# Kernel optimization log

Hardware: AMD Instinct MI355X
Metric: run time of the kernel (lower is better)

## Reference

```python
import jax, jax.numpy as jnp
import numpy as np

N_SRC1, N_DST1, N_DST2 = 200000, 50000, 10000
E1, E2 = 2000000, 400000
IN_F, H_F, N_CLS = 128, 256, 47


def setup_inputs() -> dict:
    key = jax.random.key(0)
    ks = jax.random.split(key, 10)
    x = jax.random.normal(ks[0], (N_SRC1, IN_F), dtype=jnp.float32)
    W_self1 = jax.random.normal(ks[1], (IN_F, H_F), dtype=jnp.float32) * (1.0 / np.sqrt(IN_F))
    W_neigh1 = jax.random.normal(ks[2], (IN_F, H_F), dtype=jnp.float32) * (1.0 / np.sqrt(IN_F))
    b1 = jnp.zeros((H_F,), dtype=jnp.float32)
    W_self2 = jax.random.normal(ks[3], (H_F, N_CLS), dtype=jnp.float32) * (1.0 / np.sqrt(H_F))
    W_neigh2 = jax.random.normal(ks[4], (H_F, N_CLS), dtype=jnp.float32) * (1.0 / np.sqrt(H_F))
    b2 = jnp.zeros((N_CLS,), dtype=jnp.float32)
    src1 = jax.random.randint(ks[5], (E1,), 0, N_SRC1, dtype=jnp.int64)
    dst1 = jnp.sort(jax.random.randint(ks[6], (E1,), 0, N_DST1, dtype=jnp.int64))
    src2 = jax.random.randint(ks[7], (E2,), 0, N_DST1, dtype=jnp.int64)
    dst2 = jnp.sort(jax.random.randint(ks[8], (E2,), 0, N_DST2, dtype=jnp.int64))
    return {"x": x, "W_self1": W_self1, "W_neigh1": W_neigh1, "b1": b1,
            "W_self2": W_self2, "W_neigh2": W_neigh2, "b2": b2,
            "src1": src1, "dst1": dst1, "src2": src2, "dst2": dst2,
            "n_dst1": N_DST1, "n_dst2": N_DST2}


def _sage_mean(h_src, h_dst, src, dst, n_dst, W_self, W_neigh, b):
    # mean neighbor aggregation: gather src feats, segment-sum onto dst, divide by in-degree
    msum = jax.ops.segment_sum(h_src[src], dst, num_segments=n_dst)  # [n_dst, F]
    deg = jax.ops.segment_sum(jnp.ones(src.shape, h_src.dtype), dst, num_segments=n_dst)
    h_neigh = msum / jnp.maximum(deg, 1.0)[:, None]
    return h_dst @ W_self + h_neigh @ W_neigh + b


def reference(x, W_self1, W_neigh1, b1, W_self2, W_neigh2, b2,
              src1, dst1, src2, dst2, n_dst1, n_dst2):
    # layer 1 (dst nodes are the prefix of src nodes, DGL MFG convention)
    h = _sage_mean(x, x[:n_dst1], src1, dst1, n_dst1, W_self1, W_neigh1, b1)
    h = jax.nn.relu(h)  # dropout = identity (eval mode)
    # layer 2
    out = _sage_mean(h, h[:n_dst2], src2, dst2, n_dst2, W_self2, W_neigh2, b2)
    return out
```

## Files before the change

kernel.cpp:

```cpp
#include <hip/hip_runtime.h>

constexpr int N_DST1 = 50000;
constexpr int N_DST2 = 10000;
constexpr int E1     = 2000000;
constexpr int E2     = 400000;
constexpr int IN_F   = 128;
constexpr int H_F    = 256;
constexpr int N_CLS  = 47;

constexpr size_t RP1_OFF = 0;
constexpr size_t RP2_OFF = 204800;
constexpr size_t BPS_OFF = 245760;
constexpr size_t BPN_OFF = 311296;
constexpr size_t BP2_OFF = 376832;
constexpr size_t X8_OFF  = 430080;
constexpr size_t HN1_OFF = 26030080;
constexpr size_t HB_OFF  = 38830080;
constexpr size_t H8_OFF  = 64430080;
constexpr size_t HN2_OFF = 77230080;

using f32x4  = __attribute__((ext_vector_type(4))) float;
using f32x2  = __attribute__((ext_vector_type(2))) float;
using short8 = __attribute__((ext_vector_type(8))) short;

__device__ __forceinline__ ushort f2bf(float f) {
    union { float f; unsigned u; } v; v.f = f;
    unsigned u = v.u;
    return (ushort)((u + 0x7fffu + ((u >> 16) & 1u)) >> 16);
}

constexpr int CAST_BLKS = 200000 * IN_F / 8 / 256;
constexpr int PACK_BLKS = 44;
constexpr int RP_BLKS   = (N_DST1 + N_DST2 + 2 + 255) / 256;

__global__ __launch_bounds__(256) void setup_all(
    const float* __restrict__ x, unsigned char* __restrict__ x8,
    const float* __restrict__ Ws1, const float* __restrict__ Wn1,
    const float* __restrict__ Ws2, const float* __restrict__ Wn2,
    ushort* __restrict__ bps, ushort* __restrict__ bpn, ushort* __restrict__ bp2,
    const int* __restrict__ dst1, const int* __restrict__ dst2,
    int* __restrict__ rp1, int* __restrict__ rp2) {
    int b = blockIdx.x;
    if (b < CAST_BLKS) {
        int i = b * 256 + threadIdx.x;
        float4 v0 = ((const float4*)x)[2 * i];
        float4 v1 = ((const float4*)x)[2 * i + 1];
        int p0 = __builtin_amdgcn_cvt_pk_fp8_f32(v0.x, v0.y, 0, false);
        p0     = __builtin_amdgcn_cvt_pk_fp8_f32(v0.z, v0.w, p0, true);
        int p1 = __builtin_amdgcn_cvt_pk_fp8_f32(v1.x, v1.y, 0, false);
        p1     = __builtin_amdgcn_cvt_pk_fp8_f32(v1.z, v1.w, p1, true);
        uint2 o; o.x = (unsigned)p0; o.y = (unsigned)p1;
        ((uint2*)x8)[i] = o;
    } else if (b < CAST_BLKS + PACK_BLKS) {
        int pb = b - CAST_BLKS;
        if (pb < 32) {
            const float* W = (pb < 16) ? Ws1 : Wn1;
            ushort* P      = (pb < 16) ? bps : bpn;
            int idx = (pb & 15) * 256 + threadIdx.x;
            int lane = idx & 63, kb = (idx >> 6) & 3, nb = idx >> 8;
            int n  = nb * 16 + (lane & 15);
            int k0 = kb * 32 + ((lane >> 4) * 8);
            ushort tmp[8];
#pragma unroll
            for (int j = 0; j < 8; ++j) tmp[j] = f2bf(W[(k0 + j) * H_F + n]);
            ((uint4*)P)[idx] = *(uint4*)tmp;
        } else {
            int idx = (pb - 32) * 256 + threadIdx.x;
            if (idx < 3072) {
                int lane = idx & 63, rem = idx >> 6;
                int nb = rem % 3, kb = rem / 3;
                int col = nb * 16 + (lane & 15);
                int k0  = (kb & 7) * 32 + ((lane >> 4) * 8);
                const float* W = (kb < 8) ? Ws2 : Wn2;
                ushort tmp[8];
#pragma unroll
                for (int j = 0; j < 8; ++j)
                    tmp[j] = (col < N_CLS) ? f2bf(W[(k0 + j) * N_CLS + col]) : (ushort)0;
                ((uint4*)bp2)[(kb * 3 + nb) * 64 + lane] = *(uint4*)tmp;
            }
        }
    } else {
        int idx = (b - CAST_BLKS - PACK_BLKS) * 256 + threadIdx.x;
        const int* dst; int* rp; int E; int target;
        if (idx <= N_DST1) { dst = dst1; rp = rp1; E = E1; target = idx; }
        else if (idx <= N_DST1 + 1 + N_DST2) {
            dst = dst2; rp = rp2; E = E2; target = idx - (N_DST1 + 1);
        } else return;
        int lo = 0, hi = E;
        while (lo < hi) {
            int mid = (lo + hi) >> 1;
            if (dst[mid] < target) lo = mid + 1; else hi = mid;
        }
        rp[target] = lo;
    }
}

__global__ __launch_bounds__(256) void agg1b(const unsigned char* __restrict__ x8,
                                             const int* __restrict__ src,
                                             const int* __restrict__ rp,
                                             ushort* __restrict__ hn) {
    int t = threadIdx.x & 63;
    int d = blockIdx.x * 4 + (threadIdx.x >> 6);
    int s = rp[d], e = rp[d + 1];
    int deg = e - s;
    const uint4* x4 = (const uint4*)x8;
    int g = t >> 3, c = t & 7;
    f32x2 a2[8] = {};
    auto accv = [&](uint4 v) {
        a2[0] += __builtin_amdgcn_cvt_pk_f32_fp8((int)v.x, false);
        a2[1] += __builtin_amdgcn_cvt_pk_f32_fp8((int)v.x, true);
        a2[2] += __builtin_amdgcn_cvt_pk_f32_fp8((int)v.y, false);
        a2[3] += __builtin_amdgcn_cvt_pk_f32_fp8((int)v.y, true);
        a2[4] += __builtin_amdgcn_cvt_pk_f32_fp8((int)v.z, false);
        a2[5] += __builtin_amdgcn_cvt_pk_f32_fp8((int)v.z, true);
        a2[6] += __builtin_amdgcn_cvt_pk_f32_fp8((int)v.w, false);
        a2[7] += __builtin_amdgcn_cvt_pk_f32_fp8((int)v.w, true);
    };
    for (int b0 = s; b0 < e; b0 += 64) {
        int nb = min(64, e - b0);
        int idx = 0;
        if (t < nb) idx = src[b0 + t];
        int nfull = nb >> 3;
        int j = 0;
        for (; j + 4 <= nfull; j += 4) {
            int e0 = __shfl(idx, (j + 0) * 8 + g);
            int e1 = __shfl(idx, (j + 1) * 8 + g);
            int e2 = __shfl(idx, (j + 2) * 8 + g);
            int e3 = __shfl(idx, (j + 3) * 8 + g);
            uint4 v0 = x4[(size_t)e0 * 8 + c];
            uint4 v1 = x4[(size_t)e1 * 8 + c];
            uint4 v2 = x4[(size_t)e2 * 8 + c];
            uint4 v3 = x4[(size_t)e3 * 8 + c];
            accv(v0); accv(v1); accv(v2); accv(v3);
        }
        for (; j < nfull; ++j) {
            int e0 = __shfl(idx, j * 8 + g);
            uint4 v = x4[(size_t)e0 * 8 + c];
            accv(v);
        }
        int rem = nb & 7;
        int er = __shfl(idx, (nfull * 8 + g) & 63);
        if (g < rem) {
            uint4 v = x4[(size_t)er * 8 + c];
            accv(v);
        }
    }
#pragma unroll
    for (int q = 0; q < 8; ++q) {
#pragma unroll
        for (int h = 0; h < 2; ++h) {
            float av = a2[q][h];
            av += __shfl_xor(av, 8);
            av += __shfl_xor(av, 16);
            av += __shfl_xor(av, 32);
            a2[q][h] = av;
        }
    }
    if (t < 8) {
        float inv = 1.f / fmaxf((float)deg, 1.f);
        unsigned o[8];
#pragma unroll
        for (int p = 0; p < 8; ++p)
            o[p] = (unsigned)f2bf(a2[p][0] * inv) |
                   ((unsigned)f2bf(a2[p][1] * inv) << 16);
        uint4* hrow = (uint4*)hn + (size_t)d * 16 + t * 2;
        hrow[0] = make_uint4(o[0], o[1], o[2], o[3]);
        hrow[1] = make_uint4(o[4], o[5], o[6], o[7]);
    }
}

__global__ __launch_bounds__(256) void agg2b(const unsigned char* __restrict__ h8,
                                             const int* __restrict__ src,
                                             const int* __restrict__ rp,
                                             ushort* __restrict__ hn) {
    int t = threadIdx.x & 63;
    int d = blockIdx.x * 4 + (threadIdx.x >> 6);
    int s = rp[d], e = rp[d + 1];
    int deg = e - s;
    const uint4* h4 = (const uint4*)h8;
    int g = t >> 4, c = t & 15;
    f32x2 a2[8] = {};
    auto accv = [&](uint4 v) {
        a2[0] += __builtin_amdgcn_cvt_pk_f32_fp8((int)v.x, false);
        a2[1] += __builtin_amdgcn_cvt_pk_f32_fp8((int)v.x, true);
        a2[2] += __builtin_amdgcn_cvt_pk_f32_fp8((int)v.y, false);
        a2[3] += __builtin_amdgcn_cvt_pk_f32_fp8((int)v.y, true);
        a2[4] += __builtin_amdgcn_cvt_pk_f32_fp8((int)v.z, false);
        a2[5] += __builtin_amdgcn_cvt_pk_f32_fp8((int)v.z, true);
        a2[6] += __builtin_amdgcn_cvt_pk_f32_fp8((int)v.w, false);
        a2[7] += __builtin_amdgcn_cvt_pk_f32_fp8((int)v.w, true);
    };
    for (int b0 = s; b0 < e; b0 += 64) {
        int nb = min(64, e - b0);
        int idx = 0;
        if (t < nb) idx = src[b0 + t];
        int nfull = nb >> 2;
        int j = 0;
        for (; j + 4 <= nfull; j += 4) {
            int e0 = __shfl(idx, (j + 0) * 4 + g);
            int e1 = __shfl(idx, (j + 1) * 4 + g);
            int e2 = __shfl(idx, (j + 2) * 4 + g);
            int e3 = __shfl(idx, (j + 3) * 4 + g);
            uint4 v0 = h4[(size_t)e0 * 16 + c];
            uint4 v1 = h4[(size_t)e1 * 16 + c];
            uint4 v2 = h4[(size_t)e2 * 16 + c];
            uint4 v3 = h4[(size_t)e3 * 16 + c];
            accv(v0); accv(v1); accv(v2); accv(v3);
        }
        for (; j < nfull; ++j) {
            int e0 = __shfl(idx, j * 4 + g);
            uint4 v = h4[(size_t)e0 * 16 + c];
            accv(v);
        }
        int rem = nb & 3;
        int er = __shfl(idx, (nfull * 4 + g) & 63);
        if (g < rem) {
            uint4 v = h4[(size_t)er * 16 + c];
            accv(v);
        }
    }
#pragma unroll
    for (int q = 0; q < 8; ++q) {
#pragma unroll
        for (int h = 0; h < 2; ++h) {
            float av = a2[q][h];
            av += __shfl_xor(av, 16);
            av += __shfl_xor(av, 32);
            a2[q][h] = av;
        }
    }
    if (t < 16) {
        float inv = 1.f / fmaxf((float)deg, 1.f);
        unsigned o[8];
#pragma unroll
        for (int p = 0; p < 8; ++p)
            o[p] = (unsigned)f2bf(a2[p][0] * inv) |
                   ((unsigned)f2bf(a2[p][1] * inv) << 16);
        uint4* hrow = (uint4*)hn + (size_t)d * 32 + t * 2;
        hrow[0] = make_uint4(o[0], o[1], o[2], o[3]);
        hrow[1] = make_uint4(o[4], o[5], o[6], o[7]);
    }
}

__global__ __launch_bounds__(256) void gemm1_mfma(
    const float* __restrict__ x, const ushort* __restrict__ hn1,
    const ushort* __restrict__ BpS, const ushort* __restrict__ BpN,
    const float* __restrict__ b1, ushort* __restrict__ hb,
    unsigned char* __restrict__ h8) {
    int tid = threadIdx.x;
    int wave = tid >> 6, lane = tid & 63;
    int m0 = blockIdx.x * 16;
    int nb0 = wave * 4;
    int mloc = lane & 15;
    int mrow = m0 + mloc;
    int koff = (lane >> 4) * 8;

    const float*  Af = x   + (size_t)mrow * IN_F;
    const ushort* Ah = hn1 + (size_t)mrow * IN_F;
    short8 a0[4], a1[4];
#pragma unroll
    for (int kb = 0; kb < 4; ++kb) {
        float4 q0 = *(const float4*)(Af + kb * 32 + koff);
        float4 q1 = *(const float4*)(Af + kb * 32 + koff + 4);
        a0[kb][0] = (short)f2bf(q0.x); a0[kb][1] = (short)f2bf(q0.y);
        a0[kb][2] = (short)f2bf(q0.z); a0[kb][3] = (short)f2bf(q0.w);
        a0[kb][4] = (short)f2bf(q1.x); a0[kb][5] = (short)f2bf(q1.y);
        a0[kb][6] = (short)f2bf(q1.z); a0[kb][7] = (short)f2bf(q1.w);
        a1[kb] = *(const short8*)(Ah + kb * 32 + koff);
    }

    f32x4 acc[4];
#pragma unroll
    for (int nb = 0; nb < 4; ++nb) acc[nb] = (f32x4){0.f, 0.f, 0.f, 0.f};

#pragma unroll
    for (int kb = 0; kb < 4; ++kb)
#pragma unroll
        for (int nb = 0; nb < 4; ++nb) {
            short8 b = *(const short8*)(BpS + ((size_t)((nb0 + nb) * 4 + kb) * 64 + lane) * 8);
            acc[nb] = __builtin_amdgcn_mfma_f32_16x16x32_bf16(a0[kb], b, acc[nb], 0, 0, 0);
        }
#pragma unroll
    for (int kb = 0; kb < 4; ++kb)
#pragma unroll
        for (int nb = 0; nb < 4; ++nb) {
            short8 b = *(const short8*)(BpN + ((size_t)((nb0 + nb) * 4 + kb) * 64 + lane) * 8);
            acc[nb] = __builtin_amdgcn_mfma_f32_16x16x32_bf16(a1[kb], b, acc[nb], 0, 0, 0);
        }

    int crow0 = m0 + (lane >> 4) * 4;
    int ccol  = lane & 15;
#pragma unroll
    for (int nb = 0; nb < 4; ++nb) {
        size_t col = (size_t)(nb0 + nb) * 16 + ccol;
        float bias = b1[col];
#pragma unroll
        for (int r = 0; r < 4; ++r) {
            int row = crow0 + r;
            float v = fmaxf(acc[nb][r] + bias, 0.f);
            int p = __builtin_amdgcn_cvt_pk_fp8_f32(v, v, 0, false);
            h8[(size_t)row * H_F + col] = (unsigned char)(p & 0xff);
            if (row < N_DST2) hb[(size_t)row * H_F + col] = f2bf(v);
        }
    }
}

__global__ __launch_bounds__(256) void gemm2_mfma(
    const ushort* __restrict__ hb, const ushort* __restrict__ hn2,
    const ushort* __restrict__ P2, const float* __restrict__ b2,
    float* __restrict__ out) {
    int tid = threadIdx.x;
    int wave = tid >> 6, lane = tid & 63;
    int m0 = (blockIdx.x * 4 + wave) * 16;
    if (m0 >= N_DST2) return;
    int mrow = m0 + (lane & 15);
    int koff = (lane >> 4) * 8;

    f32x4 acc[3];
#pragma unroll
    for (int nb = 0; nb < 3; ++nb) acc[nb] = (f32x4){0.f, 0.f, 0.f, 0.f};

#pragma unroll
    for (int kb = 0; kb < 16; ++kb) {
        const ushort* A = (kb < 8)
            ? (hb  + (size_t)mrow * H_F + kb * 32 + koff)
            : (hn2 + (size_t)mrow * H_F + (kb - 8) * 32 + koff);
        short8 a = *(const short8*)A;
#pragma unroll
        for (int nb = 0; nb < 3; ++nb) {
            short8 b = *(const short8*)(P2 + ((size_t)(kb * 3 + nb) * 64 + lane) * 8);
            acc[nb] = __builtin_amdgcn_mfma_f32_16x16x32_bf16(a, b, acc[nb], 0, 0, 0);
        }
    }
    int crow0 = m0 + (lane >> 4) * 4;
    int ccol  = lane & 15;
#pragma unroll
    for (int nb = 0; nb < 3; ++nb) {
        int col = nb * 16 + ccol;
        if (col < N_CLS) {
            float bias = b2[col];
#pragma unroll
            for (int r = 0; r < 4; ++r)
                out[(size_t)(crow0 + r) * N_CLS + col] = acc[nb][r] + bias;
        }
    }
}

extern "C" void kernel_launch(void* const* d_in, const int* in_sizes, int n_in,
                              void* d_out, int out_size, void* d_ws, size_t ws_size,
                              hipStream_t stream) {
    const float* x   = (const float*)d_in[0];
    const float* Ws1 = (const float*)d_in[1];
    const float* Wn1 = (const float*)d_in[2];
    const float* b1  = (const float*)d_in[3];
    const float* Ws2 = (const float*)d_in[4];
    const float* Wn2 = (const float*)d_in[5];
    const float* b2  = (const float*)d_in[6];
    const int* src1  = (const int*)d_in[7];
    const int* dst1  = (const int*)d_in[8];
    const int* src2  = (const int*)d_in[9];
    const int* dst2  = (const int*)d_in[10];
    float* out = (float*)d_out;

    char* ws = (char*)d_ws;
    int*           rp1 = (int*)(ws + RP1_OFF);
    int*           rp2 = (int*)(ws + RP2_OFF);
    ushort*        bps = (ushort*)(ws + BPS_OFF);
    ushort*        bpn = (ushort*)(ws + BPN_OFF);
    ushort*        bp2 = (ushort*)(ws + BP2_OFF);
    unsigned char* x8  = (unsigned char*)(ws + X8_OFF);
    ushort*        hn1 = (ushort*)(ws + HN1_OFF);
    ushort*        hb  = (ushort*)(ws + HB_OFF);
    unsigned char* h8  = (unsigned char*)(ws + H8_OFF);
    ushort*        hn2 = (ushort*)(ws + HN2_OFF);

    setup_all<<<CAST_BLKS + PACK_BLKS + RP_BLKS, 256, 0, stream>>>(
        x, x8, Ws1, Wn1, Ws2, Wn2, bps, bpn, bp2, dst1, dst2, rp1, rp2);
    agg1b<<<N_DST1 / 4, 256, 0, stream>>>(x8, src1, rp1, hn1);
    gemm1_mfma<<<N_DST1 / 16, 256, 0, stream>>>(x, hn1, bps, bpn, b1, hb, h8);
    agg2b<<<N_DST2 / 4, 256, 0, stream>>>(h8, src2, rp2, hn2);
    gemm2_mfma<<<(N_DST2 / 16 + 3) / 4, 256, 0, stream>>>(hb, hn2, bp2, b2, out);
}
```

Measured before the change: 281.7 us.

## Project layer-2 features before neighbor aggregation to shrink gather width

Uses linearity of the mean to apply W_neigh2 to every layer-1 output inside gemm1, producing a 64-wide bf16 projection per node. Layer-2 aggregation then gathers 128-byte rows instead of 256-byte fp8 rows, and gemm2 adds the aggregated projection in its epilogue instead of running a second K=256 pass. In exchange gemm1 takes on extra MFMA work, shared-memory staging and a cross-wave reduction for all 50k rows, and the projected values are rounded to bf16 before they are summed.

```diff
diff --git a/kernel.cpp b/kernel.cpp
--- a/kernel.cpp
+++ b/kernel.cpp
@@ -16,8 +16,8 @@
 constexpr size_t X8_OFF  = 430080;
 constexpr size_t HN1_OFF = 26030080;
 constexpr size_t HB_OFF  = 38830080;
-constexpr size_t H8_OFF  = 64430080;
-constexpr size_t HN2_OFF = 77230080;
+constexpr size_t Y_OFF   = 64430080;
+constexpr size_t YAGG_OFF= 77230080;
 
 using f32x4  = __attribute__((ext_vector_type(4))) float;
 using f32x2  = __attribute__((ext_vector_type(2))) float;
@@ -27,6 +27,13 @@
     union { float f; unsigned u; } v; v.f = f;
     unsigned u = v.u;
     return (ushort)((u + 0x7fffu + ((u >> 16) & 1u)) >> 16);
+}
+
+__device__ __forceinline__ float bflo(unsigned x) {
+    union { unsigned q; float f; } w; w.q = x << 16; return w.f;
+}
+__device__ __forceinline__ float bfhi(unsigned x) {
+    union { unsigned q; float f; } w; w.q = x & 0xffff0000u; return w.f;
 }
 
 constexpr int CAST_BLKS = 200000 * IN_F / 8 / 256;
@@ -169,84 +176,13 @@
     }
 }
 
-__global__ __launch_bounds__(256) void agg2b(const unsigned char* __restrict__ h8,
-                                             const int* __restrict__ src,
-                                             const int* __restrict__ rp,
-                                             ushort* __restrict__ hn) {
-    int t = threadIdx.x & 63;
-    int d = blockIdx.x * 4 + (threadIdx.x >> 6);
-    int s = rp[d], e = rp[d + 1];
-    int deg = e - s;
-    const uint4* h4 = (const uint4*)h8;
-    int g = t >> 4, c = t & 15;
-    f32x2 a2[8] = {};
-    auto accv = [&](uint4 v) {
-        a2[0] += __builtin_amdgcn_cvt_pk_f32_fp8((int)v.x, false);
-        a2[1] += __builtin_amdgcn_cvt_pk_f32_fp8((int)v.x, true);
-        a2[2] += __builtin_amdgcn_cvt_pk_f32_fp8((int)v.y, false);
-        a2[3] += __builtin_amdgcn_cvt_pk_f32_fp8((int)v.y, true);
-        a2[4] += __builtin_amdgcn_cvt_pk_f32_fp8((int)v.z, false);
-        a2[5] += __builtin_amdgcn_cvt_pk_f32_fp8((int)v.z, true);
-        a2[6] += __builtin_amdgcn_cvt_pk_f32_fp8((int)v.w, false);
-        a2[7] += __builtin_amdgcn_cvt_pk_f32_fp8((int)v.w, true);
-    };
-    for (int b0 = s; b0 < e; b0 += 64) {
-        int nb = min(64, e - b0);
-        int idx = 0;
-        if (t < nb) idx = src[b0 + t];
-        int nfull = nb >> 2;
-        int j = 0;
-        for (; j + 4 <= nfull; j += 4) {
-            int e0 = __shfl(idx, (j + 0) * 4 + g);
-            int e1 = __shfl(idx, (j + 1) * 4 + g);
-            int e2 = __shfl(idx, (j + 2) * 4 + g);
-            int e3 = __shfl(idx, (j + 3) * 4 + g);
-            uint4 v0 = h4[(size_t)e0 * 16 + c];
-            uint4 v1 = h4[(size_t)e1 * 16 + c];
-            uint4 v2 = h4[(size_t)e2 * 16 + c];
-            uint4 v3 = h4[(size_t)e3 * 16 + c];
-            accv(v0); accv(v1); accv(v2); accv(v3);
-        }
-        for (; j < nfull; ++j) {
-            int e0 = __shfl(idx, j * 4 + g);
-            uint4 v = h4[(size_t)e0 * 16 + c];
-            accv(v);
-        }
-        int rem = nb & 3;
-        int er = __shfl(idx, (nfull * 4 + g) & 63);
-        if (g < rem) {
-            uint4 v = h4[(size_t)er * 16 + c];
-            accv(v);
-        }
-    }
-#pragma unroll
-    for (int q = 0; q < 8; ++q) {
-#pragma unroll
-        for (int h = 0; h < 2; ++h) {
-            float av = a2[q][h];
-            av += __shfl_xor(av, 16);
-            av += __shfl_xor(av, 32);
-            a2[q][h] = av;
-        }
-    }
-    if (t < 16) {
-        float inv = 1.f / fmaxf((float)deg, 1.f);
-        unsigned o[8];
-#pragma unroll
-        for (int p = 0; p < 8; ++p)
-            o[p] = (unsigned)f2bf(a2[p][0] * inv) |
-                   ((unsigned)f2bf(a2[p][1] * inv) << 16);
-        uint4* hrow = (uint4*)hn + (size_t)d * 32 + t * 2;
-        hrow[0] = make_uint4(o[0], o[1], o[2], o[3]);
-        hrow[1] = make_uint4(o[4], o[5], o[6], o[7]);
-    }
-}
-
 __global__ __launch_bounds__(256) void gemm1_mfma(
     const float* __restrict__ x, const ushort* __restrict__ hn1,
     const ushort* __restrict__ BpS, const ushort* __restrict__ BpN,
-    const float* __restrict__ b1, ushort* __restrict__ hb,
-    unsigned char* __restrict__ h8) {
+    const ushort* __restrict__ P2, const float* __restrict__ b1,
+    ushort* __restrict__ hb, ushort* __restrict__ y) {
+    __shared__ ushort lh[16][264];
+    __shared__ f32x4 pred[3][3][64];
     int tid = threadIdx.x;
     int wave = tid >> 6, lane = tid & 63;
     int m0 = blockIdx.x * 16;
@@ -288,7 +224,7 @@
             acc[nb] = __builtin_amdgcn_mfma_f32_16x16x32_bf16(a1[kb], b, acc[nb], 0, 0, 0);
         }
 
-    int crow0 = m0 + (lane >> 4) * 4;
+    int crow0 = (lane >> 4) * 4;
     int ccol  = lane & 15;
 #pragma unroll
     for (int nb = 0; nb < 4; ++nb) {
@@ -298,15 +234,112 @@
         for (int r = 0; r < 4; ++r) {
             int row = crow0 + r;
             float v = fmaxf(acc[nb][r] + bias, 0.f);
-            int p = __builtin_amdgcn_cvt_pk_fp8_f32(v, v, 0, false);
-            h8[(size_t)row * H_F + col] = (unsigned char)(p & 0xff);
-            if (row < N_DST2) hb[(size_t)row * H_F + col] = f2bf(v);
-        }
+            ushort bv = f2bf(v);
+            lh[row][col] = bv;
+            if (m0 + row < N_DST2) hb[(size_t)(m0 + row) * H_F + col] = bv;
+        }
+    }
+    __syncthreads();
+
+    f32x4 acc2[3];
+#pragma unroll
+    for (int q = 0; q < 3; ++q) acc2[q] = (f32x4){0.f, 0.f, 0.f, 0.f};
+#pragma unroll
+    for (int i = 0; i < 2; ++i) {
+        int kb = wave * 2 + i;
+        short8 a = *(const short8*)&lh[mloc][kb * 32 + koff];
+#pragma unroll
+        for (int q = 0; q < 3; ++q) {
+            short8 b = *(const short8*)(P2 + ((size_t)((8 + kb) * 3 + q) * 64 + lane) * 8);
+            acc2[q] = __builtin_amdgcn_mfma_f32_16x16x32_bf16(a, b, acc2[q], 0, 0, 0);
+        }
+    }
+    if (wave != 0) {
+#pragma unroll
+        for (int q = 0; q < 3; ++q) pred[wave - 1][q][lane] = acc2[q];
+    }
+    __syncthreads();
+    if (wave == 0) {
+#pragma unroll
+        for (int q = 0; q < 3; ++q) {
+            f32x4 v = acc2[q];
+            v += pred[0][q][lane]; v += pred[1][q][lane]; v += pred[2][q][lane];
+#pragma unroll
+            for (int r = 0; r < 4; ++r)
+                y[(size_t)(m0 + crow0 + r) * 64 + q * 16 + ccol] = f2bf(v[r]);
+        }
+#pragma unroll
+        for (int r = 0; r < 4; ++r)
+            y[(size_t)(m0 + crow0 + r) * 64 + 48 + ccol] = 0;
+    }
+}
+
+__global__ __launch_bounds__(256) void agg2y(const ushort* __restrict__ y,
+                                             const int* __restrict__ src,
+                                             const int* __restrict__ rp,
+                                             float* __restrict__ yagg) {
+    int t = threadIdx.x & 63;
+    int d = blockIdx.x * 4 + (threadIdx.x >> 6);
+    int s = rp[d], e = rp[d + 1];
+    int deg = e - s;
+    const uint4* y4 = (const uint4*)y;
+    int g = t >> 3, c = t & 7;
+    float a[8] = {};
+    auto accv = [&](uint4 v) {
+        a[0] += bflo(v.x); a[1] += bfhi(v.x);
+        a[2] += bflo(v.y); a[3] += bfhi(v.y);
+        a[4] += bflo(v.z); a[5] += bfhi(v.z);
+        a[6] += bflo(v.w); a[7] += bfhi(v.w);
+    };
+    for (int b0 = s; b0 < e; b0 += 64) {
+        int nb = min(64, e - b0);
+        int idx = 0;
+        if (t < nb) idx = src[b0 + t];
+        int nfull = nb >> 3;
+        int j = 0;
+        for (; j + 4 <= nfull; j += 4) {
+            int e0 = __shfl(idx, (j + 0) * 8 + g);
+            int e1 = __shfl(idx, (j + 1) * 8 + g);
+            int e2 = __shfl(idx, (j + 2) * 8 + g);
+            int e3 = __shfl(idx, (j + 3) * 8 + g);
+            uint4 v0 = y4[(size_t)e0 * 8 + c];
+            uint4 v1 = y4[(size_t)e1 * 8 + c];
+            uint4 v2 = y4[(size_t)e2 * 8 + c];
+            uint4 v3 = y4[(size_t)e3 * 8 + c];
+            accv(v0); accv(v1); accv(v2); accv(v3);
+        }
+        for (; j < nfull; ++j) {
+            int e0 = __shfl(idx, j * 8 + g);
+            uint4 v = y4[(size_t)e0 * 8 + c];
+            accv(v);
+        }
+        int rem = nb & 7;
+        int er = __shfl(idx, (nfull * 8 + g) & 63);
+        if (g < rem) {
+            uint4 v = y4[(size_t)er * 8 + c];
+            accv(v);
+        }
+    }
+#pragma unroll
+    for (int q = 0; q < 8; ++q) {
+        float av = a[q];
+        av += __shfl_xor(av, 8);
+        av += __shfl_xor(av, 16);
+        av += __shfl_xor(av, 32);
+        a[q] = av;
+    }
+    if (t < 8) {
+        float inv = 1.f / fmaxf((float)deg, 1.f);
+        float4 o0 = make_float4(a[0] * inv, a[1] * inv, a[2] * inv, a[3] * inv);
+        float4 o1 = make_float4(a[4] * inv, a[5] * inv, a[6] * inv, a[7] * inv);
+        float4* row = (float4*)(yagg + (size_t)d * 64 + t * 8);
+        row[0] = o0;
+        row[1] = o1;
     }
 }
 
 __global__ __launch_bounds__(256) void gemm2_mfma(
-    const ushort* __restrict__ hb, const ushort* __restrict__ hn2,
+    const ushort* __restrict__ hb, const float* __restrict__ yagg,
     const ushort* __restrict__ P2, const float* __restrict__ b2,
     float* __restrict__ out) {
     int tid = threadIdx.x;
@@ -321,11 +354,8 @@
     for (int nb = 0; nb < 3; ++nb) acc[nb] = (f32x4){0.f, 0.f, 0.f, 0.f};
 
 #pragma unroll
-    for (int kb = 0; kb < 16; ++kb) {
-        const ushort* A = (kb < 8)
-            ? (hb  + (size_t)mrow * H_F + kb * 32 + koff)
-            : (hn2 + (size_t)mrow * H_F + (kb - 8) * 32 + koff);
-        short8 a = *(const short8*)A;
+    for (int kb = 0; kb < 8; ++kb) {
+        short8 a = *(const short8*)(hb + (size_t)mrow * H_F + kb * 32 + koff);
 #pragma unroll
         for (int nb = 0; nb < 3; ++nb) {
             short8 b = *(const short8*)(P2 + ((size_t)(kb * 3 + nb) * 64 + lane) * 8);
@@ -340,8 +370,10 @@
         if (col < N_CLS) {
             float bias = b2[col];
 #pragma unroll
-            for (int r = 0; r < 4; ++r)
-                out[(size_t)(crow0 + r) * N_CLS + col] = acc[nb][r] + bias;
+            for (int r = 0; r < 4; ++r) {
+                float nv = yagg[(size_t)(crow0 + r) * 64 + col];
+                out[(size_t)(crow0 + r) * N_CLS + col] = acc[nb][r] + nv + bias;
+            }
         }
     }
 }
@@ -371,13 +403,13 @@
     unsigned char* x8  = (unsigned char*)(ws + X8_OFF);
     ushort*        hn1 = (ushort*)(ws + HN1_OFF);
     ushort*        hb  = (ushort*)(ws + HB_OFF);
-    unsigned char* h8  = (unsigned char*)(ws + H8_OFF);
-    ushort*        hn2 = (ushort*)(ws + HN2_OFF);
+    ushort*        y   = (ushort*)(ws + Y_OFF);
+    float*         yagg= (float*)(ws + YAGG_OFF);
 
     setup_all<<<CAST_BLKS + PACK_BLKS + RP_BLKS, 256, 0, stream>>>(
         x, x8, Ws1, Wn1, Ws2, Wn2, bps, bpn, bp2, dst1, dst2, rp1, rp2);
     agg1b<<<N_DST1 / 4, 256, 0, stream>>>(x8, src1, rp1, hn1);
-    gemm1_mfma<<<N_DST1 / 16, 256, 0, stream>>>(x, hn1, bps, bpn, b1, hb, h8);
-    agg2b<<<N_DST2 / 4, 256, 0, stream>>>(h8, src2, rp2, hn2);
-    gemm2_mfma<<<(N_DST2 / 16 + 3) / 4, 256, 0, stream>>>(hb, hn2, bp2, b2, out);
-}
+    gemm1_mfma<<<N_DST1 / 16, 256, 0, stream>>>(x, hn1, bps, bpn, bp2, b1, hb, y);
+    agg2y<<<N_DST2 / 4, 256, 0, stream>>>(y, src2, rp2, yagg);
+    gemm2_mfma<<<(N_DST2 / 16 + 3) / 4, 256, 0, stream>>>(hb, yagg, bp2, b2, out);
+}
```

Result: faster. 276.0 us (-2.0%).
